# Performance work log

Measured on AMD Instinct MI355X. Metric: run time of the kernel, lower is better.

The kernel has to match this reference:

```python
import jax, jax.numpy as jnp
import numpy as np

DIM = 2048
N_HEAD = 32
N_KV_HEAD = 8
HEAD_DIM = DIM // N_HEAD  # 64
BSZ = 2
SEQ = 2048


def apply_rotary_emb(x, freqs_cis):
    # x: [b, s, h, d]; freqs_cis: [s, d//2, 2]
    xs = x.reshape(*x.shape[:-1], -1, 2)          # [b, s, h, d//2, 2]
    fc = freqs_cis.reshape(1, xs.shape[1], 1, xs.shape[3], 2)
    x0, x1 = xs[..., 0], xs[..., 1]
    c, s = fc[..., 0], fc[..., 1]
    out = jnp.stack([x0 * c - x1 * s, x1 * c + x0 * s], axis=-1)
    return out.reshape(x.shape).astype(x.dtype)


def setup_inputs() -> dict:
    key = jax.random.key(0)
    k1, k2, k3, k4 = jax.random.split(key, 4)
    x = jax.random.normal(k1, (BSZ, SEQ, DIM), dtype=jnp.float32)
    # rotary cos/sin table [seq, head_dim//2, 2]
    theta = 1.0 / (10000.0 ** (jnp.arange(0, HEAD_DIM, 2, dtype=jnp.float32) / HEAD_DIM))
    ang = jnp.arange(SEQ, dtype=jnp.float32)[:, None] * theta[None, :]
    freqs_cis = jnp.stack([jnp.cos(ang), jnp.sin(ang)], axis=-1)
    mask = jnp.tril(jnp.ones((SEQ, SEQ), dtype=bool))  # causal
    scale = 0.02
    wqkv = jax.random.normal(k2, ((N_HEAD + 2 * N_KV_HEAD) * HEAD_DIM, DIM), dtype=jnp.float32) * scale
    wo = jax.random.normal(k3, (DIM, DIM), dtype=jnp.float32) * scale
    return {"x": x, "freqs_cis": freqs_cis, "mask": mask, "wqkv": wqkv, "wo": wo}


def reference(x, freqs_cis, mask, wqkv, wo):
    bsz, seqlen, _ = x.shape
    kv_size = N_KV_HEAD * HEAD_DIM
    qkv = x @ wqkv.T  # [b, s, dim + 2*kv]
    xq, xk, xv = jnp.split(qkv, [DIM, DIM + kv_size], axis=-1)
    xq = xq.reshape(bsz, seqlen, N_HEAD, HEAD_DIM)
    xk = xk.reshape(bsz, seqlen, N_KV_HEAD, HEAD_DIM)
    xv = xv.reshape(bsz, seqlen, N_KV_HEAD, HEAD_DIM)
    xq = apply_rotary_emb(xq, freqs_cis)
    xk = apply_rotary_emb(xk, freqs_cis)
    # [b, h, s, d]
    xq = xq.transpose(0, 2, 1, 3)
    xk = xk.transpose(0, 2, 1, 3)
    xv = xv.transpose(0, 2, 1, 3)
    rep = N_HEAD // N_KV_HEAD
    keys = jnp.repeat(xk, rep, axis=1)
    values = jnp.repeat(xv, rep, axis=1)
    scores = jnp.einsum("bhqd,bhkd->bhqk", xq, keys) / np.sqrt(HEAD_DIM).astype(np.float32)
    scores = jnp.where(mask, scores, jnp.finfo(scores.dtype).min)
    attn = jax.nn.softmax(scores, axis=-1)
    out = jnp.einsum("bhqk,bhkd->bhqd", attn, values)
    out = out.transpose(0, 2, 1, 3).reshape(bsz, seqlen, DIM)
    return out @ wo.T
```

## Files before the change

kernel.cpp:

```cpp
#include <hip/hip_runtime.h>
#include <hip/hip_bf16.h>

typedef __attribute__((ext_vector_type(8))) short short8;
typedef __attribute__((ext_vector_type(4))) short short4v;
typedef __attribute__((ext_vector_type(4))) float f32x4;
typedef __hip_bfloat16 bf16;

#define SEQ 2048
#define DIM 2048
#define NH 32
#define NKV 8
#define HD 64
#define QKVD 3072
#define KVD 512
#define SMSCALE 0.18033688011112042f

__device__ inline void gld_lds16(const bf16* g, bf16* l) {
    __builtin_amdgcn_global_load_lds((const __attribute__((address_space(1))) void*)g,
                                     (__attribute__((address_space(3))) void*)l, 16, 0, 0);
}

__device__ inline void store_val(float* p, float v) { *p = v; }
__device__ inline void store_val(bf16* p, float v) { *p = __float2bfloat16(v); }

__device__ inline unsigned pkbf16(float a, float b) {
    __hip_bfloat162 h = __float22bfloat162_rn(make_float2(a, b));
    return *(unsigned*)&h;
}

__device__ inline float b2f(short x) {
    unsigned u = (unsigned)(unsigned short)x << 16;
    union { unsigned u; float f; } c; c.u = u; return c.f;
}

__global__ void cvt3_kernel(const float* __restrict__ x, const float* __restrict__ wqkv,
                            const float* __restrict__ wo, bf16* __restrict__ out) {
    int i = blockIdx.x * blockDim.x + threadIdx.x;
    const float* src; int off;
    if (i < 2097152) { src = x; off = i; }
    else if (i < 3670016) { src = wqkv; off = i - 2097152; }
    else { src = wo; off = i - 3670016; }
    float4 v = ((const float4*)src)[off];
    uint2 u;
    u.x = pkbf16(v.x, v.y);
    u.y = pkbf16(v.z, v.w);
    ((uint2*)out)[i] = u;
}

template <typename CT>
__global__ __launch_bounds__(256, 3) void gemm_nt(const bf16* __restrict__ A,
                                                  const bf16* __restrict__ Bt,
                                                  CT* __restrict__ C,
                                                  int M, int N, int K) {
    __shared__ bf16 As[128 * 32];
    __shared__ bf16 Bs[128 * 32];
    const int tid = threadIdx.x;
    const int lane = tid & 63;
    const int quad = lane >> 4;
    const int r16 = lane & 15;
    const int wave = tid >> 6;
    const int bm = blockIdx.y * 128;
    const int bn = blockIdx.x * 128;
    const int wm = (wave >> 1) * 64;
    const int wn = (wave & 1) * 64;

    f32x4 acc[4][4] = {};

    const int arow = tid >> 2;
    const int kch = (tid & 3) * 8;
    const bf16* Ap = A + (size_t)(bm + arow) * K + kch;
    const bf16* Bp = Bt + (size_t)(bn + arow) * K + kch;
    bf16* Asd = As + tid * 8;
    bf16* Bsd = Bs + tid * 8;
    const int kq = quad * 8;

    for (int k0 = 0; k0 < K; k0 += 32) {
        __syncthreads();
        gld_lds16(Ap, Asd);
        gld_lds16(Ap + (size_t)64 * K, Asd + 64 * 32);
        gld_lds16(Bp, Bsd);
        gld_lds16(Bp + (size_t)64 * K, Bsd + 64 * 32);
        Ap += 32; Bp += 32;
        __syncthreads();
        short8 af[4], bfr[4];
#pragma unroll
        for (int i = 0; i < 4; i++)
            af[i] = *(const short8*)(As + (wm + i * 16 + r16) * 32 + kq);
#pragma unroll
        for (int j = 0; j < 4; j++)
            bfr[j] = *(const short8*)(Bs + (wn + j * 16 + r16) * 32 + kq);
#pragma unroll
        for (int i = 0; i < 4; i++)
#pragma unroll
            for (int j = 0; j < 4; j++)
                acc[i][j] = __builtin_amdgcn_mfma_f32_16x16x32_bf16(af[i], bfr[j], acc[i][j], 0, 0, 0);
    }
#pragma unroll
    for (int i = 0; i < 4; i++)
#pragma unroll
        for (int j = 0; j < 4; j++) {
            int row = bm + wm + i * 16 + quad * 4;
            int col = bn + wn + j * 16 + r16;
#pragma unroll
            for (int r = 0; r < 4; r++)
                store_val(C + (size_t)(row + r) * N + col, acc[i][j][r]);
        }
}

__global__ void rope_qk_kernel(const bf16* __restrict__ qkv, const float* __restrict__ fc,
                               bf16* __restrict__ qr, bf16* __restrict__ kr) {
    const int row = blockIdx.y;
    const int s = row & (SEQ - 1);
    const int col = (blockIdx.x * 64 + threadIdx.x) * 8;
    const bf16* src = qkv + (size_t)row * QKVD + col;
    short8 v = *(const short8*)src;
    const int j0 = (col & 63) >> 1;
    const float4* fcp = (const float4*)(fc + ((size_t)s * 32 + j0) * 2);
    float4 f01 = fcp[0];
    float4 f23 = fcp[1];

    bf16* dst;
    float sc;
    if (col < DIM) { dst = qr + (size_t)row * DIM + col; sc = SMSCALE; }
    else           { dst = kr + (size_t)row * KVD + (col - DIM); sc = 1.0f; }

    float x0 = b2f(v[0]), x1 = b2f(v[1]), x2 = b2f(v[2]), x3 = b2f(v[3]);
    float x4 = b2f(v[4]), x5 = b2f(v[5]), x6 = b2f(v[6]), x7 = b2f(v[7]);
    float c0 = f01.x * sc, s0 = f01.y * sc, c1 = f01.z * sc, s1 = f01.w * sc;
    float c2 = f23.x * sc, s2 = f23.y * sc, c3 = f23.z * sc, s3 = f23.w * sc;

    uint4 o;
    o.x = pkbf16(x0 * c0 - x1 * s0, x1 * c0 + x0 * s0);
    o.y = pkbf16(x2 * c1 - x3 * s1, x3 * c1 + x2 * s1);
    o.z = pkbf16(x4 * c2 - x5 * s2, x5 * c2 + x4 * s2);
    o.w = pkbf16(x6 * c3 - x7 * s3, x7 * c3 + x6 * s3);
    *(uint4*)dst = o;
}

__global__ void rope_v_kernel(const bf16* __restrict__ qkv, bf16* __restrict__ vt) {
    const int t = threadIdx.x;
    const int so = t & 63;
    const int dq = t >> 6;
    const int bk = blockIdx.y;
    const int s = blockIdx.x * 64 + so;
    const int b = bk >> 3;
    const bf16* src = qkv + ((size_t)b * SEQ + s) * QKVD + DIM + KVD + (bk & 7) * HD + dq * 16;
    short8 v0 = *(const short8*)src;
    short8 v1 = *(const short8*)(src + 8);
    short* dst = (short*)(vt + ((size_t)bk * HD + dq * 16) * SEQ + s);
#pragma unroll
    for (int j = 0; j < 8; j++) dst[(size_t)j * SEQ] = v0[j];
#pragma unroll
    for (int j = 0; j < 8; j++) dst[(size_t)(8 + j) * SEQ] = v1[j];
}

__global__ __launch_bounds__(256, 4) void attn_kernel(const bf16* __restrict__ qr,
                                                      const bf16* __restrict__ kr,
                                                      const bf16* __restrict__ vt,
                                                      bf16* __restrict__ out) {
    __shared__ bf16 Ks[8192];
    __shared__ bf16 Vs[8192];
    const int t = threadIdx.x;
    const int lane = t & 63;
    const int wv = t >> 6;
    const int quad = lane >> 4;
    const int r16 = lane & 15;

    const int wg = blockIdx.x;
    const int xcd = wg & 7;
    const int kk = wg >> 3;
    const int bk = xcd * 2 + (kk & 1);
    const int qt = 127 - (kk >> 1);
    const int b = bk >> 3;
    const int kvh = bk & 7;
    const int h = kvh * 4 + wv;
    const int q0 = qt * 16;
    const int nkb = (qt >> 2) + 1;

    const bf16* Kg = kr + ((size_t)b * SEQ + lane) * KVD + kvh * HD + wv * 8;
    const bf16* Vg = vt + ((size_t)(b * NKV + kvh) * HD + lane) * SEQ + wv * 8;

    const char* kl = (const char*)Ks + quad * 1024 + r16 * 16;
    const char* vl = (const char*)Vs + (quad >> 1) * 1024 + r16 * 16 + (quad & 1) * 8;

    union PB { short4v s; unsigned u[2]; };

    const short one_bf16 = (short)0x3F80;
    const short4v ones = {one_bf16, one_bf16, one_bf16, one_bf16};

    const bf16* Qp = qr + ((size_t)b * SEQ + q0 + r16) * DIM + h * HD + quad * 8;
    short8 qa0 = *(const short8*)(Qp);
    short8 qa1 = *(const short8*)(Qp + 32);

    f32x4 o[4] = {};
    f32x4 o_l = {};

    {
        bf16* Ksd = Ks + t * 8;
        bf16* Vsd = Vs + t * 8;
        gld_lds16(Kg, Ksd);      gld_lds16(Kg + 32, Ksd + 2048);
        gld_lds16(Vg, Vsd);      gld_lds16(Vg + 32, Vsd + 2048);
    }

    for (int kb = 0; kb < nkb; kb++) {
        __syncthreads();
        const int buf = kb & 1;
        if (kb + 1 < nkb) {
            const bf16* Kgn = Kg + (size_t)(kb + 1) * 64 * KVD;
            const bf16* Vgn = Vg + (kb + 1) * 64;
            bf16* Ksd = Ks + (buf ^ 1) * 4096 + t * 8;
            bf16* Vsd = Vs + (buf ^ 1) * 4096 + t * 8;
            gld_lds16(Kgn, Ksd);      gld_lds16(Kgn + 32, Ksd + 2048);
            gld_lds16(Vgn, Vsd);      gld_lds16(Vgn + 32, Vsd + 2048);
        }
        const char* klb = kl + buf * 8192;
        const char* vlb = vl + buf * 8192;

        const f32x4 z = {0.f, 0.f, 0.f, 0.f};
        f32x4 st[4];
        __builtin_amdgcn_s_setprio(1);
#pragma unroll
        for (int n = 0; n < 4; n++) {
            short8 kf0 = *(const short8*)(klb + n * 256);
            short8 kf1 = *(const short8*)(klb + 4096 + n * 256);
            st[n] = __builtin_amdgcn_mfma_f32_16x16x32_bf16(kf0, qa0, z, 0, 0, 0);
            st[n] = __builtin_amdgcn_mfma_f32_16x16x32_bf16(kf1, qa1, st[n], 0, 0, 0);
        }
        __builtin_amdgcn_s_setprio(0);

        short4v vf[4][4];
#pragma unroll
        for (int dt = 0; dt < 4; dt++)
#pragma unroll
            for (int n = 0; n < 4; n++)
                vf[dt][n] = *(const short4v*)(vlb + n * 2048 + dt * 256);
        __builtin_amdgcn_sched_barrier(0);

        if (kb == nkb - 1) {
            const int kbase = kb * 64;
#pragma unroll
            for (int n = 0; n < 4; n++)
#pragma unroll
                for (int r = 0; r < 4; r++) {
                    int key = kbase + n * 16 + quad * 4 + r;
                    if (key > q0 + r16) st[n][r] = -__builtin_inff();
                }
        }

        PB pbs[4];
#pragma unroll
        for (int n = 0; n < 4; n++) {
            float p0 = exp2f(st[n][0]);
            float p1 = exp2f(st[n][1]);
            float p2 = exp2f(st[n][2]);
            float p3 = exp2f(st[n][3]);
            pbs[n].u[0] = pkbf16(p0, p1);
            pbs[n].u[1] = pkbf16(p2, p3);
        }

        __builtin_amdgcn_s_setprio(1);
#pragma unroll
        for (int dt = 0; dt < 4; dt++)
#pragma unroll
            for (int n = 0; n < 4; n++)
                o[dt] = __builtin_amdgcn_mfma_f32_16x16x16bf16_1k(vf[dt][n], pbs[n].s, o[dt], 0, 0, 0);
#pragma unroll
        for (int n = 0; n < 4; n++)
            o_l = __builtin_amdgcn_mfma_f32_16x16x16bf16_1k(ones, pbs[n].s, o_l, 0, 0, 0);
        __builtin_amdgcn_s_setprio(0);
    }

    float inv_l = 1.f / o_l[0];
    bf16* Op = out + ((size_t)b * SEQ + q0 + r16) * DIM + h * HD + quad * 4;
#pragma unroll
    for (int dt = 0; dt < 4; dt++) {
        PB pk;
        pk.u[0] = pkbf16(o[dt][0] * inv_l, o[dt][1] * inv_l);
        pk.u[1] = pkbf16(o[dt][2] * inv_l, o[dt][3] * inv_l);
        *(short4v*)(Op + dt * 16) = pk.s;
    }
}

extern "C" void kernel_launch(void* const* d_in, const int* in_sizes, int n_in,
                              void* d_out, int out_size, void* d_ws, size_t ws_size,
                              hipStream_t stream) {
    (void)in_sizes; (void)n_in; (void)out_size; (void)ws_size;
    const float* x    = (const float*)d_in[0];
    const float* fc   = (const float*)d_in[1];
    const float* wqkv = (const float*)d_in[3];
    const float* wo   = (const float*)d_in[4];
    float* out = (float*)d_out;

    char* w = (char*)d_ws;
    bf16* xb    = (bf16*)(w);
    bf16* wqkvb = (bf16*)(w + 16777216);
    bf16* wob   = (bf16*)(w + 29360128);
    bf16* qkvb  = (bf16*)(w + 37748736);
    bf16* kr    = (bf16*)(w + 62914560);
    bf16* vt    = (bf16*)(w + 67108864);
    bf16* qr = xb;
    bf16* attnb = qkvb;

    cvt3_kernel<<<18432, 256, 0, stream>>>(x, wqkv, wo, xb);
    gemm_nt<bf16><<<dim3(24, 32), 256, 0, stream>>>(xb, wqkvb, qkvb, 4096, QKVD, DIM);
    rope_qk_kernel<<<dim3(5, 4096), 64, 0, stream>>>(qkvb, fc, qr, kr);
    rope_v_kernel<<<dim3(32, 16), 256, 0, stream>>>(qkvb, vt);
    attn_kernel<<<dim3(2048), 256, 0, stream>>>(qr, kr, vt, attnb);
    gemm_nt<float><<<dim3(16, 32), 256, 0, stream>>>(attnb, wob, out, 4096, DIM, DIM);
}
```

Baseline: 326.2 us.

## Replace GEMMs with 256x256 double-buffered 8-wave pipelined kernel

Both projection GEMMs move from a 128x128 single-buffered kernel to a 256x256 tile with 8 waves, BK=64, and double-buffered LDS filled by direct global-to-LDS loads. The loads are spread across four MFMA phases, using partial vmcnt waits, barriers and setprio, so global fetches overlap compute. LDS addresses are XOR-swizzled to avoid bank conflicts. The cost is fewer blocks (192 and 128 workgroups on a large-CU GPU), which risks under-filling the machine, plus 128KB of LDS per block.

```diff
diff --git a/kernel.cpp b/kernel.cpp
--- a/kernel.cpp
+++ b/kernel.cpp
@@ -48,63 +48,146 @@
 }
 
 template <typename CT>
-__global__ __launch_bounds__(256, 3) void gemm_nt(const bf16* __restrict__ A,
-                                                  const bf16* __restrict__ Bt,
-                                                  CT* __restrict__ C,
-                                                  int M, int N, int K) {
-    __shared__ bf16 As[128 * 32];
-    __shared__ bf16 Bs[128 * 32];
+__global__ __launch_bounds__(512, 2) void gemm8p(const bf16* __restrict__ A,
+                                                 const bf16* __restrict__ Bt,
+                                                 CT* __restrict__ C,
+                                                 int N, int K) {
+    __shared__ bf16 Abuf[2][16384];
+    __shared__ bf16 Bbuf[2][16384];
     const int tid = threadIdx.x;
     const int lane = tid & 63;
     const int quad = lane >> 4;
     const int r16 = lane & 15;
-    const int wave = tid >> 6;
-    const int bm = blockIdx.y * 128;
-    const int bn = blockIdx.x * 128;
-    const int wm = (wave >> 1) * 64;
-    const int wn = (wave & 1) * 64;
-
-    f32x4 acc[4][4] = {};
-
-    const int arow = tid >> 2;
-    const int kch = (tid & 3) * 8;
-    const bf16* Ap = A + (size_t)(bm + arow) * K + kch;
-    const bf16* Bp = Bt + (size_t)(bn + arow) * K + kch;
-    bf16* Asd = As + tid * 8;
-    bf16* Bsd = Bs + tid * 8;
-    const int kq = quad * 8;
-
-    for (int k0 = 0; k0 < K; k0 += 32) {
-        __syncthreads();
-        gld_lds16(Ap, Asd);
-        gld_lds16(Ap + (size_t)64 * K, Asd + 64 * 32);
-        gld_lds16(Bp, Bsd);
-        gld_lds16(Bp + (size_t)64 * K, Bsd + 64 * 32);
-        Ap += 32; Bp += 32;
-        __syncthreads();
-        short8 af[4], bfr[4];
+    const int wv = tid >> 6;
+    const int wm = wv >> 2;
+    const int wn = wv & 3;
+    const int bm = blockIdx.y * 256;
+    const int bn = blockIdx.x * 256;
+    const int swz = (lane & 7) * 8;
+
+    const int sc = (((tid & 7) ^ ((tid >> 3) & 7)) * 8);
+    const bf16* Ap = A + (size_t)(bm + (tid >> 3)) * K + sc;
+    const bf16* Bp = Bt + (size_t)(bn + (tid >> 3)) * K + sc;
+
+    f32x4 acc[8][4] = {};
+    const int NT = K >> 6;
+
+    {
+        bf16* Ad = &Abuf[0][0] + tid * 8;
+        bf16* Bd = &Bbuf[0][0] + tid * 8;
+        gld_lds16(Ap, Ad);                          gld_lds16(Ap + (size_t)64 * K, Ad + 4096);
+        gld_lds16(Bp, Bd);                          gld_lds16(Bp + (size_t)64 * K, Bd + 4096);
+        gld_lds16(Ap + (size_t)128 * K, Ad + 8192); gld_lds16(Ap + (size_t)192 * K, Ad + 12288);
+        gld_lds16(Bp + (size_t)128 * K, Bd + 8192); gld_lds16(Bp + (size_t)192 * K, Bd + 12288);
+    }
+    asm volatile("s_waitcnt vmcnt(0)" ::: "memory");
+    __builtin_amdgcn_s_barrier();
+
+    short8 af[4][2], af2[4][2], bf0[2][2], bf1[2][2];
+
+#define GPH_MID \
+    asm volatile("s_waitcnt vmcnt(4)" ::: "memory"); \
+    __builtin_amdgcn_s_barrier(); \
+    asm volatile("s_waitcnt lgkmcnt(0)" ::: "memory"); \
+    __builtin_amdgcn_s_setprio(1)
+#define GPH_END \
+    __builtin_amdgcn_s_setprio(0); \
+    __builtin_amdgcn_s_barrier()
+#define MFMA_BF16(a, b, c) __builtin_amdgcn_mfma_f32_16x16x32_bf16(a, b, c, 0, 0, 0)
+
+#pragma unroll 1
+    for (int t = 0; t < NT; t++) {
+        const bf16* Ac = &Abuf[t & 1][0];
+        const bf16* Bc = &Bbuf[t & 1][0];
+        bf16* Ad = &Abuf[(t & 1) ^ 1][0] + tid * 8;
+        bf16* Bd = &Bbuf[(t & 1) ^ 1][0] + tid * 8;
+        const bf16* Apn = Ap + (size_t)(t + 1) * 64;
+        const bf16* Bpn = Bp + (size_t)(t + 1) * 64;
+        const bool stg = (t + 1 < NT);
+
+#pragma unroll
+        for (int i = 0; i < 4; i++) {
+            const bf16* p = Ac + (wm * 64 + i * 16 + r16) * 64;
+            af[i][0] = *(const short8*)(p + ((quad * 8) ^ swz));
+            af[i][1] = *(const short8*)(p + ((32 + quad * 8) ^ swz));
+        }
+#pragma unroll
+        for (int j = 0; j < 2; j++) {
+            const bf16* p = Bc + (wn * 32 + j * 16 + r16) * 64;
+            bf0[j][0] = *(const short8*)(p + ((quad * 8) ^ swz));
+            bf0[j][1] = *(const short8*)(p + ((32 + quad * 8) ^ swz));
+        }
+        if (stg) { gld_lds16(Apn, Ad); gld_lds16(Apn + (size_t)64 * K, Ad + 4096); }
+        GPH_MID;
 #pragma unroll
         for (int i = 0; i < 4; i++)
-            af[i] = *(const short8*)(As + (wm + i * 16 + r16) * 32 + kq);
-#pragma unroll
-        for (int j = 0; j < 4; j++)
-            bfr[j] = *(const short8*)(Bs + (wn + j * 16 + r16) * 32 + kq);
+#pragma unroll
+            for (int j = 0; j < 2; j++) {
+                acc[i][j] = MFMA_BF16(af[i][0], bf0[j][0], acc[i][j]);
+                acc[i][j] = MFMA_BF16(af[i][1], bf0[j][1], acc[i][j]);
+            }
+        GPH_END;
+
+#pragma unroll
+        for (int i = 0; i < 4; i++) {
+            const bf16* p = Ac + (128 + wm * 64 + i * 16 + r16) * 64;
+            af2[i][0] = *(const short8*)(p + ((quad * 8) ^ swz));
+            af2[i][1] = *(const short8*)(p + ((32 + quad * 8) ^ swz));
+        }
+        if (stg) { gld_lds16(Bpn, Bd); gld_lds16(Bpn + (size_t)64 * K, Bd + 4096); }
+        GPH_MID;
 #pragma unroll
         for (int i = 0; i < 4; i++)
 #pragma unroll
-            for (int j = 0; j < 4; j++)
-                acc[i][j] = __builtin_amdgcn_mfma_f32_16x16x32_bf16(af[i], bfr[j], acc[i][j], 0, 0, 0);
-    }
-#pragma unroll
-    for (int i = 0; i < 4; i++)
+            for (int j = 0; j < 2; j++) {
+                acc[4 + i][j] = MFMA_BF16(af2[i][0], bf0[j][0], acc[4 + i][j]);
+                acc[4 + i][j] = MFMA_BF16(af2[i][1], bf0[j][1], acc[4 + i][j]);
+            }
+        GPH_END;
+
+#pragma unroll
+        for (int j = 0; j < 2; j++) {
+            const bf16* p = Bc + (128 + wn * 32 + j * 16 + r16) * 64;
+            bf1[j][0] = *(const short8*)(p + ((quad * 8) ^ swz));
+            bf1[j][1] = *(const short8*)(p + ((32 + quad * 8) ^ swz));
+        }
+        if (stg) { gld_lds16(Apn + (size_t)128 * K, Ad + 8192); gld_lds16(Apn + (size_t)192 * K, Ad + 12288); }
+        GPH_MID;
+#pragma unroll
+        for (int i = 0; i < 4; i++)
+#pragma unroll
+            for (int j = 0; j < 2; j++) {
+                acc[4 + i][2 + j] = MFMA_BF16(af2[i][0], bf1[j][0], acc[4 + i][2 + j]);
+                acc[4 + i][2 + j] = MFMA_BF16(af2[i][1], bf1[j][1], acc[4 + i][2 + j]);
+            }
+        GPH_END;
+
+        if (stg) { gld_lds16(Bpn + (size_t)128 * K, Bd + 8192); gld_lds16(Bpn + (size_t)192 * K, Bd + 12288); }
+        GPH_MID;
+#pragma unroll
+        for (int i = 0; i < 4; i++)
+#pragma unroll
+            for (int j = 0; j < 2; j++) {
+                acc[i][2 + j] = MFMA_BF16(af[i][0], bf1[j][0], acc[i][2 + j]);
+                acc[i][2 + j] = MFMA_BF16(af[i][1], bf1[j][1], acc[i][2 + j]);
+            }
+        GPH_END;
+    }
+
+#pragma unroll
+    for (int i = 0; i < 8; i++) {
+        int row = bm + (i < 4 ? wm * 64 + i * 16 : 128 + wm * 64 + (i - 4) * 16) + quad * 4;
 #pragma unroll
         for (int j = 0; j < 4; j++) {
-            int row = bm + wm + i * 16 + quad * 4;
-            int col = bn + wn + j * 16 + r16;
+            int col = bn + wn * 32 + (j < 2 ? j * 16 : 128 + (j - 2) * 16) + r16;
 #pragma unroll
             for (int r = 0; r < 4; r++)
                 store_val(C + (size_t)(row + r) * N + col, acc[i][j][r]);
         }
+    }
+#undef GPH_MID
+#undef GPH_END
+#undef MFMA_BF16
 }
 
 __global__ void rope_qk_kernel(const bf16* __restrict__ qkv, const float* __restrict__ fc,
@@ -302,9 +385,9 @@
     bf16* attnb = qkvb;
 
     cvt3_kernel<<<18432, 256, 0, stream>>>(x, wqkv, wo, xb);
-    gemm_nt<bf16><<<dim3(24, 32), 256, 0, stream>>>(xb, wqkvb, qkvb, 4096, QKVD, DIM);
+    gemm8p<bf16><<<dim3(12, 16), 512, 0, stream>>>(xb, wqkvb, qkvb, QKVD, DIM);
     rope_qk_kernel<<<dim3(5, 4096), 64, 0, stream>>>(qkvb, fc, qr, kr);
     rope_v_kernel<<<dim3(32, 16), 256, 0, stream>>>(qkvb, vt);
     attn_kernel<<<dim3(2048), 256, 0, stream>>>(qr, kr, vt, attnb);
-    gemm_nt<float><<<dim3(16, 32), 256, 0, stream>>>(attnb, wob, out, 4096, DIM, DIM);
-}
+    gemm8p<float><<<dim3(8, 16), 512, 0, stream>>>(attnb, wob, out, DIM, DIM);
+}
```

New measurement: 335.0 us. 1.03x slower.

## Replace QKV projection GEMM with 256x256-tile 8-wave double-buffered pipelined kernel

Applied to the files above, without the earlier changes.

Adds a new bf16 GEMM kernel using 256x256 output tiles, 512 threads, double-buffered LDS filled by direct global-to-LDS loads with an XOR swizzle, and staged vmcnt waits so loads for the next K-tile overlap MFMA work on the current one. Only the QKV projection switches to it; the output projection keeps the old GEMM. The grid shrinks to 192 blocks, which gives more reuse per tile but fewer workgroups than the GPU has CUs, and the interleaved barrier and prefetch schedule adds complexity.

```diff
diff --git a/kernel.cpp b/kernel.cpp
--- a/kernel.cpp
+++ b/kernel.cpp
@@ -107,6 +107,143 @@
         }
 }
 
+template <typename CT>
+__global__ __launch_bounds__(512, 2) void gemm8p(const bf16* __restrict__ A,
+                                                 const bf16* __restrict__ Bt,
+                                                 CT* __restrict__ C,
+                                                 int N, int K) {
+    __shared__ bf16 Abuf[2][16384];
+    __shared__ bf16 Bbuf[2][16384];
+    const int tid = threadIdx.x;
+    const int lane = tid & 63;
+    const int quad = lane >> 4;
+    const int r16 = lane & 15;
+    const int wv = tid >> 6;
+    const int wm = wv >> 2;
+    const int wn = wv & 3;
+    const int bm = blockIdx.y * 256;
+    const int bn = blockIdx.x * 256;
+    const int swz = (lane & 7) * 8;
+
+    const int sc = (((tid & 7) ^ ((tid >> 3) & 7)) * 8);
+    const bf16* Ap = A + (size_t)(bm + (tid >> 3)) * K + sc;
+    const bf16* Bp = Bt + (size_t)(bn + (tid >> 3)) * K + sc;
+
+    f32x4 acc[8][4] = {};
+    const int NT = K >> 6;
+
+    {
+        bf16* Ad = &Abuf[0][0] + tid * 8;
+        bf16* Bd = &Bbuf[0][0] + tid * 8;
+        gld_lds16(Ap, Ad);                          gld_lds16(Ap + (size_t)64 * K, Ad + 4096);
+        gld_lds16(Bp, Bd);                          gld_lds16(Bp + (size_t)64 * K, Bd + 4096);
+        gld_lds16(Bp + (size_t)128 * K, Bd + 8192); gld_lds16(Bp + (size_t)192 * K, Bd + 12288);
+        gld_lds16(Ap + (size_t)128 * K, Ad + 8192); gld_lds16(Ap + (size_t)192 * K, Ad + 12288);
+    }
+
+    short8 af[4][2], af2[4][2], bf0[2][2], bf1[2][2];
+
+#define VMW(nstr) asm volatile("s_waitcnt vmcnt(" nstr ")" ::: "memory")
+#define BARF() { __builtin_amdgcn_s_barrier(); __builtin_amdgcn_sched_barrier(0); }
+#define RD_AF(dst, rbase)                                                     \
+    _Pragma("unroll")                                                         \
+    for (int i = 0; i < 4; i++) {                                             \
+        const bf16* p = Ac + ((rbase) + wm * 64 + i * 16 + r16) * 64;         \
+        dst[i][0] = *(const short8*)(p + ((quad * 8) ^ swz));                 \
+        dst[i][1] = *(const short8*)(p + ((32 + quad * 8) ^ swz));            \
+    }
+#define RD_BF(dst, rbase)                                                     \
+    _Pragma("unroll")                                                         \
+    for (int j = 0; j < 2; j++) {                                             \
+        const bf16* p = Bc + ((rbase) + wn * 32 + j * 16 + r16) * 64;         \
+        dst[j][0] = *(const short8*)(p + ((quad * 8) ^ swz));                 \
+        dst[j][1] = *(const short8*)(p + ((32 + quad * 8) ^ swz));            \
+    }
+#define MFMA_BF16(a, b, c) __builtin_amdgcn_mfma_f32_16x16x32_bf16(a, b, c, 0, 0, 0)
+#define MFMAQ(ai, bj, io, jo)                                                 \
+    __builtin_amdgcn_s_setprio(1);                                            \
+    _Pragma("unroll")                                                         \
+    for (int i = 0; i < 4; i++)                                               \
+        _Pragma("unroll")                                                     \
+        for (int j = 0; j < 2; j++) {                                         \
+            acc[(io) + i][(jo) + j] = MFMA_BF16(ai[i][0], bj[j][0], acc[(io) + i][(jo) + j]); \
+            acc[(io) + i][(jo) + j] = MFMA_BF16(ai[i][1], bj[j][1], acc[(io) + i][(jo) + j]); \
+        }                                                                     \
+    __builtin_amdgcn_s_setprio(0);
+
+#pragma unroll 1
+    for (int t = 0; t < NT - 1; t++) {
+        const int bi = t & 1;
+        const bf16* Ac = &Abuf[bi][0];
+        const bf16* Bc = &Bbuf[bi][0];
+        bf16* Ad = &Abuf[bi ^ 1][0] + tid * 8;
+        bf16* Bd = &Bbuf[bi ^ 1][0] + tid * 8;
+        const bf16* Apn = Ap + (size_t)(t + 1) * 64;
+        const bf16* Bpn = Bp + (size_t)(t + 1) * 64;
+
+        gld_lds16(Apn, Ad); gld_lds16(Apn + (size_t)64 * K, Ad + 4096);
+        VMW("6");
+        BARF();
+        RD_AF(af, 0)
+        RD_BF(bf0, 0)
+        MFMAQ(af, bf0, 0, 0)
+
+        gld_lds16(Bpn, Bd); gld_lds16(Bpn + (size_t)64 * K, Bd + 4096);
+        VMW("6");
+        BARF();
+        RD_BF(bf1, 128)
+        MFMAQ(af, bf1, 0, 2)
+
+        gld_lds16(Bpn + (size_t)128 * K, Bd + 8192); gld_lds16(Bpn + (size_t)192 * K, Bd + 12288);
+        VMW("6");
+        BARF();
+        RD_AF(af2, 128)
+        MFMAQ(af2, bf1, 4, 2)
+        BARF();
+
+        gld_lds16(Apn + (size_t)128 * K, Ad + 8192); gld_lds16(Apn + (size_t)192 * K, Ad + 12288);
+        MFMAQ(af2, bf0, 4, 0)
+    }
+
+    {
+        const int bi = (NT - 1) & 1;
+        const bf16* Ac = &Abuf[bi][0];
+        const bf16* Bc = &Bbuf[bi][0];
+        VMW("4");
+        BARF();
+        RD_AF(af, 0)
+        RD_BF(bf0, 0)
+        MFMAQ(af, bf0, 0, 0)
+        VMW("2");
+        BARF();
+        RD_BF(bf1, 128)
+        MFMAQ(af, bf1, 0, 2)
+        VMW("0");
+        BARF();
+        RD_AF(af2, 128)
+        MFMAQ(af2, bf1, 4, 2)
+        MFMAQ(af2, bf0, 4, 0)
+    }
+
+#pragma unroll
+    for (int i = 0; i < 8; i++) {
+        int row = bm + (i < 4 ? wm * 64 + i * 16 : 128 + wm * 64 + (i - 4) * 16) + quad * 4;
+#pragma unroll
+        for (int j = 0; j < 4; j++) {
+            int col = bn + wn * 32 + (j < 2 ? j * 16 : 128 + (j - 2) * 16) + r16;
+#pragma unroll
+            for (int r = 0; r < 4; r++)
+                store_val(C + (size_t)(row + r) * N + col, acc[i][j][r]);
+        }
+    }
+#undef VMW
+#undef BARF
+#undef RD_AF
+#undef RD_BF
+#undef MFMA_BF16
+#undef MFMAQ
+}
+
 __global__ void rope_qk_kernel(const bf16* __restrict__ qkv, const float* __restrict__ fc,
                                bf16* __restrict__ qr, bf16* __restrict__ kr) {
     const int row = blockIdx.y;
@@ -302,7 +439,7 @@
     bf16* attnb = qkvb;
 
     cvt3_kernel<<<18432, 256, 0, stream>>>(x, wqkv, wo, xb);
-    gemm_nt<bf16><<<dim3(24, 32), 256, 0, stream>>>(xb, wqkvb, qkvb, 4096, QKVD, DIM);
+    gemm8p<bf16><<<dim3(12, 16), 512, 0, stream>>>(xb, wqkvb, qkvb, QKVD, DIM);
     rope_qk_kernel<<<dim3(5, 4096), 64, 0, stream>>>(qkvb, fc, qr, kr);
     rope_v_kernel<<<dim3(32, 16), 256, 0, stream>>>(qkvb, vt);
     attn_kernel<<<dim3(2048), 256, 0, stream>>>(qr, kr, vt, attnb);
```

Result: no change. 331.8 us (+1.7%).

## Process two 16-row query tiles per wave and pair causal tiles per block

Applied to the files above, without the earlier changes.

Each wave now handles 32 query rows (two 16-row MFMA tiles), so every K/V tile loaded into LDS is reused twice. Each workgroup also processes a complementary pair of query tiles (short and long causal lengths), which balances work across blocks. The grid shrinks from 2048 to 512 blocks and launch bounds drop to 2 waves per SIMD to leave room for the extra accumulator registers. The costs are lower occupancy, fewer blocks to spread over the CUs, and the serial two-segment loop inside each block.

```diff
diff --git a/kernel.cpp b/kernel.cpp
--- a/kernel.cpp
+++ b/kernel.cpp
@@ -154,7 +154,7 @@
     for (int j = 0; j < 8; j++) dst[(size_t)(8 + j) * SEQ] = v1[j];
 }
 
-__global__ __launch_bounds__(256, 4) void attn_kernel(const bf16* __restrict__ qr,
+__global__ __launch_bounds__(256, 2) void attn_kernel(const bf16* __restrict__ qr,
                                                       const bf16* __restrict__ kr,
                                                       const bf16* __restrict__ vt,
                                                       bf16* __restrict__ out) {
@@ -170,12 +170,10 @@
     const int xcd = wg & 7;
     const int kk = wg >> 3;
     const int bk = xcd * 2 + (kk & 1);
-    const int qt = 127 - (kk >> 1);
+    const int pairIdx = kk >> 1;
     const int b = bk >> 3;
     const int kvh = bk & 7;
     const int h = kvh * 4 + wv;
-    const int q0 = qt * 16;
-    const int nkb = (qt >> 2) + 1;
 
     const bf16* Kg = kr + ((size_t)b * SEQ + lane) * KVD + kvh * HD + wv * 8;
     const bf16* Vg = vt + ((size_t)(b * NKV + kvh) * HD + lane) * SEQ + wv * 8;
@@ -184,100 +182,124 @@
     const char* vl = (const char*)Vs + (quad >> 1) * 1024 + r16 * 16 + (quad & 1) * 8;
 
     union PB { short4v s; unsigned u[2]; };
-
     const short one_bf16 = (short)0x3F80;
     const short4v ones = {one_bf16, one_bf16, one_bf16, one_bf16};
 
-    const bf16* Qp = qr + ((size_t)b * SEQ + q0 + r16) * DIM + h * HD + quad * 8;
-    short8 qa0 = *(const short8*)(Qp);
-    short8 qa1 = *(const short8*)(Qp + 32);
-
-    f32x4 o[4] = {};
-    f32x4 o_l = {};
-
-    {
-        bf16* Ksd = Ks + t * 8;
-        bf16* Vsd = Vs + t * 8;
-        gld_lds16(Kg, Ksd);      gld_lds16(Kg + 32, Ksd + 2048);
-        gld_lds16(Vg, Vsd);      gld_lds16(Vg + 32, Vsd + 2048);
-    }
-
-    for (int kb = 0; kb < nkb; kb++) {
+#pragma unroll 1
+    for (int seg = 0; seg < 2; seg++) {
+        const int qt = seg ? (63 - pairIdx) : pairIdx;
+        const int q0 = qt * 32;
+        const int nkb = (qt >> 1) + 1;
+
+        const bf16* QpA = qr + ((size_t)b * SEQ + q0 + r16) * DIM + h * HD + quad * 8;
+        const bf16* QpB = QpA + (size_t)16 * DIM;
+        short8 qaA0 = *(const short8*)(QpA);
+        short8 qaA1 = *(const short8*)(QpA + 32);
+        short8 qaB0 = *(const short8*)(QpB);
+        short8 qaB1 = *(const short8*)(QpB + 32);
+
+        f32x4 oA[4] = {}, oB[4] = {};
+        f32x4 olA = {}, olB = {};
+
         __syncthreads();
-        const int buf = kb & 1;
-        if (kb + 1 < nkb) {
-            const bf16* Kgn = Kg + (size_t)(kb + 1) * 64 * KVD;
-            const bf16* Vgn = Vg + (kb + 1) * 64;
-            bf16* Ksd = Ks + (buf ^ 1) * 4096 + t * 8;
-            bf16* Vsd = Vs + (buf ^ 1) * 4096 + t * 8;
-            gld_lds16(Kgn, Ksd);      gld_lds16(Kgn + 32, Ksd + 2048);
-            gld_lds16(Vgn, Vsd);      gld_lds16(Vgn + 32, Vsd + 2048);
+        {
+            bf16* Ksd = Ks + t * 8;
+            bf16* Vsd = Vs + t * 8;
+            gld_lds16(Kg, Ksd);      gld_lds16(Kg + 32, Ksd + 2048);
+            gld_lds16(Vg, Vsd);      gld_lds16(Vg + 32, Vsd + 2048);
         }
-        const char* klb = kl + buf * 8192;
-        const char* vlb = vl + buf * 8192;
-
-        const f32x4 z = {0.f, 0.f, 0.f, 0.f};
-        f32x4 st[4];
-        __builtin_amdgcn_s_setprio(1);
-#pragma unroll
-        for (int n = 0; n < 4; n++) {
-            short8 kf0 = *(const short8*)(klb + n * 256);
-            short8 kf1 = *(const short8*)(klb + 4096 + n * 256);
-            st[n] = __builtin_amdgcn_mfma_f32_16x16x32_bf16(kf0, qa0, z, 0, 0, 0);
-            st[n] = __builtin_amdgcn_mfma_f32_16x16x32_bf16(kf1, qa1, st[n], 0, 0, 0);
+
+        for (int kb = 0; kb < nkb; kb++) {
+            __syncthreads();
+            const int buf = kb & 1;
+            if (kb + 1 < nkb) {
+                const bf16* Kgn = Kg + (size_t)(kb + 1) * 64 * KVD;
+                const bf16* Vgn = Vg + (kb + 1) * 64;
+                bf16* Ksd = Ks + (buf ^ 1) * 4096 + t * 8;
+                bf16* Vsd = Vs + (buf ^ 1) * 4096 + t * 8;
+                gld_lds16(Kgn, Ksd);      gld_lds16(Kgn + 32, Ksd + 2048);
+                gld_lds16(Vgn, Vsd);      gld_lds16(Vgn + 32, Vsd + 2048);
+            }
+            const char* klb = kl + buf * 8192;
+            const char* vlb = vl + buf * 8192;
+
+            const f32x4 z = {0.f, 0.f, 0.f, 0.f};
+            f32x4 stA[4], stB[4];
+            __builtin_amdgcn_s_setprio(1);
+#pragma unroll
+            for (int n = 0; n < 4; n++) {
+                short8 kf0 = *(const short8*)(klb + n * 256);
+                short8 kf1 = *(const short8*)(klb + 4096 + n * 256);
+                stA[n] = __builtin_amdgcn_mfma_f32_16x16x32_bf16(kf0, qaA0, z, 0, 0, 0);
+                stA[n] = __builtin_amdgcn_mfma_f32_16x16x32_bf16(kf1, qaA1, stA[n], 0, 0, 0);
+                stB[n] = __builtin_amdgcn_mfma_f32_16x16x32_bf16(kf0, qaB0, z, 0, 0, 0);
+                stB[n] = __builtin_amdgcn_mfma_f32_16x16x32_bf16(kf1, qaB1, stB[n], 0, 0, 0);
+            }
+            __builtin_amdgcn_s_setprio(0);
+
+            short4v vf[4][4];
+#pragma unroll
+            for (int dt = 0; dt < 4; dt++)
+#pragma unroll
+                for (int n = 0; n < 4; n++)
+                    vf[dt][n] = *(const short4v*)(vlb + n * 2048 + dt * 256);
+            __builtin_amdgcn_sched_barrier(0);
+
+            if (kb == nkb - 1) {
+                const int kbase = kb * 64;
+#pragma unroll
+                for (int n = 0; n < 4; n++)
+#pragma unroll
+                    for (int r = 0; r < 4; r++) {
+                        int key = kbase + n * 16 + quad * 4 + r;
+                        if (key > q0 + r16) stA[n][r] = -__builtin_inff();
+                        if (key > q0 + 16 + r16) stB[n][r] = -__builtin_inff();
+                    }
+            }
+
+            PB pbsA[4], pbsB[4];
+#pragma unroll
+            for (int n = 0; n < 4; n++) {
+                float a0 = exp2f(stA[n][0]), a1 = exp2f(stA[n][1]);
+                float a2 = exp2f(stA[n][2]), a3 = exp2f(stA[n][3]);
+                pbsA[n].u[0] = pkbf16(a0, a1);
+                pbsA[n].u[1] = pkbf16(a2, a3);
+                float b0 = exp2f(stB[n][0]), b1 = exp2f(stB[n][1]);
+                float b2 = exp2f(stB[n][2]), b3 = exp2f(stB[n][3]);
+                pbsB[n].u[0] = pkbf16(b0, b1);
+                pbsB[n].u[1] = pkbf16(b2, b3);
+            }
+
+            __builtin_amdgcn_s_setprio(1);
+#pragma unroll
+            for (int dt = 0; dt < 4; dt++)
+#pragma unroll
+                for (int n = 0; n < 4; n++) {
+                    oA[dt] = __builtin_amdgcn_mfma_f32_16x16x16bf16_1k(vf[dt][n], pbsA[n].s, oA[dt], 0, 0, 0);
+                    oB[dt] = __builtin_amdgcn_mfma_f32_16x16x16bf16_1k(vf[dt][n], pbsB[n].s, oB[dt], 0, 0, 0);
+                }
+#pragma unroll
+            for (int n = 0; n < 4; n++) {
+                olA = __builtin_amdgcn_mfma_f32_16x16x16bf16_1k(ones, pbsA[n].s, olA, 0, 0, 0);
+                olB = __builtin_amdgcn_mfma_f32_16x16x16bf16_1k(ones, pbsB[n].s, olB, 0, 0, 0);
+            }
+            __builtin_amdgcn_s_setprio(0);
         }
-        __builtin_amdgcn_s_setprio(0);
-
-        short4v vf[4][4];
-#pragma unroll
-        for (int dt = 0; dt < 4; dt++)
-#pragma unroll
-            for (int n = 0; n < 4; n++)
-                vf[dt][n] = *(const short4v*)(vlb + n * 2048 + dt * 256);
-        __builtin_amdgcn_sched_barrier(0);
-
-        if (kb == nkb - 1) {
-            const int kbase = kb * 64;
-#pragma unroll
-            for (int n = 0; n < 4; n++)
-#pragma unroll
-                for (int r = 0; r < 4; r++) {
-                    int key = kbase + n * 16 + quad * 4 + r;
-                    if (key > q0 + r16) st[n][r] = -__builtin_inff();
-                }
+
+        float invA = 1.f / olA[0];
+        float invB = 1.f / olB[0];
+        bf16* OpA = out + ((size_t)b * SEQ + q0 + r16) * DIM + h * HD + quad * 4;
+        bf16* OpB = OpA + (size_t)16 * DIM;
+#pragma unroll
+        for (int dt = 0; dt < 4; dt++) {
+            PB pka, pkb;
+            pka.u[0] = pkbf16(oA[dt][0] * invA, oA[dt][1] * invA);
+            pka.u[1] = pkbf16(oA[dt][2] * invA, oA[dt][3] * invA);
+            *(short4v*)(OpA + dt * 16) = pka.s;
+            pkb.u[0] = pkbf16(oB[dt][0] * invB, oB[dt][1] * invB);
+            pkb.u[1] = pkbf16(oB[dt][2] * invB, oB[dt][3] * invB);
+            *(short4v*)(OpB + dt * 16) = pkb.s;
         }
-
-        PB pbs[4];
-#pragma unroll
-        for (int n = 0; n < 4; n++) {
-            float p0 = exp2f(st[n][0]);
-            float p1 = exp2f(st[n][1]);
-            float p2 = exp2f(st[n][2]);
-            float p3 = exp2f(st[n][3]);
-            pbs[n].u[0] = pkbf16(p0, p1);
-            pbs[n].u[1] = pkbf16(p2, p3);
-        }
-
-        __builtin_amdgcn_s_setprio(1);
-#pragma unroll
-        for (int dt = 0; dt < 4; dt++)
-#pragma unroll
-            for (int n = 0; n < 4; n++)
-                o[dt] = __builtin_amdgcn_mfma_f32_16x16x16bf16_1k(vf[dt][n], pbs[n].s, o[dt], 0, 0, 0);
-#pragma unroll
-        for (int n = 0; n < 4; n++)
-            o_l = __builtin_amdgcn_mfma_f32_16x16x16bf16_1k(ones, pbs[n].s, o_l, 0, 0, 0);
-        __builtin_amdgcn_s_setprio(0);
-    }
-
-    float inv_l = 1.f / o_l[0];
-    bf16* Op = out + ((size_t)b * SEQ + q0 + r16) * DIM + h * HD + quad * 4;
-#pragma unroll
-    for (int dt = 0; dt < 4; dt++) {
-        PB pk;
-        pk.u[0] = pkbf16(o[dt][0] * inv_l, o[dt][1] * inv_l);
-        pk.u[1] = pkbf16(o[dt][2] * inv_l, o[dt][3] * inv_l);
-        *(short4v*)(Op + dt * 16) = pk.s;
     }
 }
 
@@ -305,6 +327,6 @@
     gemm_nt<bf16><<<dim3(24, 32), 256, 0, stream>>>(xb, wqkvb, qkvb, 4096, QKVD, DIM);
     rope_qk_kernel<<<dim3(5, 4096), 64, 0, stream>>>(qkvb, fc, qr, kr);
     rope_v_kernel<<<dim3(32, 16), 256, 0, stream>>>(qkvb, vt);
-    attn_kernel<<<dim3(2048), 256, 0, stream>>>(qr, kr, vt, attnb);
+    attn_kernel<<<dim3(512), 256, 0, stream>>>(qr, kr, vt, attnb);
     gemm_nt<float><<<dim3(16, 32), 256, 0, stream>>>(attnb, wob, out, 4096, DIM, DIM);
 }
```

Measured after the change: 326.2 us. No clear change (-0.0%).
